# Kernel optimization log

Measured on AMD Instinct MI355X. Metric: run time of the kernel, lower is better.

## Reference

```python
import jax, jax.numpy as jnp
import numpy as np

N, T, HW = 32, 46, 128
VOCAB_Q, NUM_ANS = 96, 32
WVEC, RNN_DIM = 32, 128
CNN_DIM, G_DIM, F_DIM = 24, 256, 256
G_IN = 2 * (CNN_DIM + 2) + RNN_DIM  # 180
BN_EPS = 1e-5


def setup_inputs() -> dict:
    key = jax.random.key(0)
    ks = jax.random.split(key, 16)
    s = 0.05
    rn = lambda k, shape: jax.random.normal(k, shape, dtype=jnp.float32) * s
    z = lambda shape: jnp.zeros(shape, jnp.float32)
    o = lambda shape: jnp.ones(shape, jnp.float32)
    inp = {}
    inp['questions'] = jax.random.randint(ks[0], (N, T), 1, VOCAB_Q)  # no NULL padding -> last step is the valid hidden state
    inp['images'] = jax.random.normal(ks[1], (N, 3, HW, HW), dtype=jnp.float32)
    inp['embed_W'] = rn(ks[2], (VOCAB_Q, WVEC))
    inp['lstm_Wih'] = rn(ks[3], (4 * RNN_DIM, WVEC))
    inp['lstm_Whh'] = rn(ks[4], (4 * RNN_DIM, RNN_DIM))
    inp['lstm_bih'] = z((4 * RNN_DIM,))
    inp['lstm_bhh'] = z((4 * RNN_DIM,))
    inp['conv0_W'] = rn(ks[5], (CNN_DIM, 3, 3, 3))
    inp['conv0_b'] = z((CNN_DIM,))
    inp['bn0_g'] = o((CNN_DIM,))
    inp['bn0_b'] = z((CNN_DIM,))
    inp['convs_W'] = rn(ks[6], (3, CNN_DIM, CNN_DIM, 3, 3))
    inp['convs_b'] = z((3, CNN_DIM))
    inp['bns_g'] = o((3, CNN_DIM))
    inp['bns_b'] = z((3, CNN_DIM))
    inp['g0_W'] = rn(ks[7], (G_DIM, G_IN))
    inp['g0_b'] = z((G_DIM,))
    inp['gs_W'] = rn(ks[8], (3, G_DIM, G_DIM))
    inp['gs_b'] = z((3, G_DIM))
    inp['f0_W'] = rn(ks[9], (F_DIM, G_DIM))
    inp['f0_b'] = z((F_DIM,))
    inp['f1_W'] = rn(ks[10], (F_DIM, F_DIM))
    inp['f1_b'] = z((F_DIM,))
    inp['f2_W'] = rn(ks[11], (NUM_ANS, F_DIM))
    inp['f2_b'] = z((NUM_ANS,))
    return inp


def _dense(x, W, b):
    return x @ W.T + b


def _lstm_last(emb, Wih, Whh, bih, bhh):
    # emb: (N, T, D); single-layer LSTM, PyTorch gate order (i, f, g, o); return last hidden state
    n, h = emb.shape[0], Whh.shape[1]
    bias = bih + bhh

    def step(carry, x_t):
        hp, cp = carry
        zg = x_t @ Wih.T + hp @ Whh.T + bias
        i, f, g, o_ = jnp.split(zg, 4, axis=-1)
        c = jax.nn.sigmoid(f) * cp + jax.nn.sigmoid(i) * jnp.tanh(g)
        hn = jax.nn.sigmoid(o_) * jnp.tanh(c)
        return (hn, c), None

    init = (jnp.zeros((n, h), emb.dtype), jnp.zeros((n, h), emb.dtype))
    (h_last, _), _ = jax.lax.scan(step, init, jnp.swapaxes(emb, 0, 1))
    return h_last


def _conv_bn_relu(x, W, b, gamma, beta):
    # Conv2d(k=3, s=2, p=1) + BatchNorm2d (training-mode batch stats) + ReLU
    x = jax.lax.conv_general_dilated(x, W, window_strides=(2, 2), padding=((1, 1), (1, 1)),
                                     dimension_numbers=('NCHW', 'OIHW', 'NCHW'))
    x = x + b[None, :, None, None]
    mu = x.mean((0, 2, 3), keepdims=True)
    var = ((x - mu) ** 2).mean((0, 2, 3), keepdims=True)  # biased var, as torch BN
    x = (x - mu) * jax.lax.rsqrt(var + BN_EPS)
    x = x * gamma[None, :, None, None] + beta[None, :, None, None]
    return jax.nn.relu(x)


def _forward(questions, images, embed_W, lstm_Wih, lstm_Whh, lstm_bih, lstm_bhh,
             conv0_W, conv0_b, bn0_g, bn0_b, convs_W, convs_b, bns_g, bns_b,
             g0_W, g0_b, gs_W, gs_b, f0_W, f0_b, f1_W, f1_b, f2_W, f2_b):
    # question encoder
    q_feats = _lstm_last(embed_W[questions], lstm_Wih, lstm_Whh, lstm_bih, lstm_bhh)  # (N, rnn_dim)
    # CNN stem
    x = _conv_bn_relu(images, conv0_W, conv0_b, bn0_g, bn0_b)
    for i in range(3):
        x = _conv_bn_relu(x, convs_W[i], convs_b[i], bns_g[i], bns_b[i])
    n, c, h, w = x.shape
    m = h * w
    # append normalized coordinates
    xc = jnp.broadcast_to(jnp.linspace(0.0, 1.0, w, dtype=x.dtype).reshape(1, 1, 1, w), (n, 1, h, w))
    yc = jnp.broadcast_to(jnp.linspace(0.0, 1.0, h, dtype=x.dtype).reshape(1, 1, h, 1), (n, 1, h, w))
    objects = jnp.concatenate([x, xc, yc], axis=1).reshape(n, c + 2, m)
    objects = jnp.swapaxes(objects, 1, 2)  # (N, M, C+2)
    # all M^2 ordered pairs: pairs[n, i*M+j] = [obj_i, obj_j]
    feats1 = jnp.repeat(objects, m, axis=1)        # (N, M^2, C+2)
    feats2 = jnp.tile(objects, (1, m, 1))          # (N, M^2, C+2)
    q_rep = jnp.broadcast_to(q_feats[:, None, :], (n, m * m, q_feats.shape[-1]))
    g_in = jnp.concatenate([feats1, feats2, q_rep], axis=-1)  # (N, M^2, 180)
    # shared MLP g
    hidden = jax.nn.relu(_dense(g_in, g0_W, g0_b))
    for i in range(3):
        hidden = jax.nn.relu(_dense(hidden, gs_W[i], gs_b[i]))
    f_in = hidden.sum(axis=1)  # old-torch sum(1) kept dim then [:,0] -> (N, g_dim)
    # MLP f (dropout = identity at eval)
    hidden = jax.nn.relu(_dense(f_in, f0_W, f0_b))
    hidden = jax.nn.relu(_dense(hidden, f1_W, f1_b))
    return _dense(hidden, f2_W, f2_b)  # (N, num_answers)


def reference(questions, images, embed_W, lstm_Wih, lstm_Whh, lstm_bih, lstm_bhh,
              conv0_W, conv0_b, bn0_g, bn0_b, convs_W, convs_b, bns_g, bns_b,
              g0_W, g0_b, gs_W, gs_b, f0_W, f0_b, f1_W, f1_b, f2_W, f2_b):
    return _forward(questions, images, embed_W, lstm_Wih, lstm_Whh, lstm_bih, lstm_bhh,
                    conv0_W, conv0_b, bn0_g, bn0_b, convs_W, convs_b, bns_g, bns_b,
                    g0_W, g0_b, gs_W, gs_b, f0_W, f0_b, f1_W, f1_b, f2_W, f2_b)
```

## Files before the change

### kernel.cpp

```cpp
#include <hip/hip_runtime.h>

#define NB   32
#define TT   46
#define RNN  128
#define CDIM 24
#define GD   256
#define GIN  180

typedef __attribute__((ext_vector_type(8))) short  bf16x8;
typedef __attribute__((ext_vector_type(4))) short  s16x4;
typedef __attribute__((ext_vector_type(8))) unsigned short u16x8;
typedef __attribute__((ext_vector_type(4))) float  f32x4;

__device__ __forceinline__ unsigned short f2bf(float v) {
    unsigned u = __float_as_uint(v);
    u = u + 0x7fffu + ((u >> 16) & 1u);
    return (unsigned short)(u >> 16);
}

__device__ __forceinline__ float fast_sigmoid(float x) {
    return 1.f / (1.f + __expf(-x));
}
__device__ __forceinline__ float fast_tanh(float x) {
    return 1.f - 2.f / (__expf(2.f * x) + 1.f);
}

__device__ __forceinline__ void lstm_body(
    const int* __restrict__ q, const float* __restrict__ embW,
    const float* __restrict__ Wih, const float* __restrict__ Whh,
    const float* __restrict__ bih, const float* __restrict__ bhh,
    float* __restrict__ qf, int n)
{
    const int tid = threadIdx.x;
    __shared__ __align__(16) float xs[32], hs[RNN];
    __shared__ float zg[512];
    f32x4 wih[8], whh[32];
    {
        const f32x4* wp = (const f32x4*)(Wih + tid * 32);
#pragma unroll
        for (int j = 0; j < 8; j++) wih[j] = wp[j];
        const f32x4* hp = (const f32x4*)(Whh + tid * RNN);
#pragma unroll
        for (int j = 0; j < 32; j++) whh[j] = hp[j];
    }
    const float bias = bih[tid] + bhh[tid];
    float creg = 0.f;
    if (tid < RNN) hs[tid] = 0.f;
    float xr = (tid < 32) ? embW[q[n * TT] * 32 + tid] : 0.f;
    __syncthreads();
    for (int t = 0; t < TT; t++) {
        if (tid < 32) xs[tid] = xr;
        __syncthreads();
        if (tid < 32 && t + 1 < TT) xr = embW[q[n * TT + t + 1] * 32 + tid];
        const f32x4* h4 = (const f32x4*)hs;
        const f32x4* x4 = (const f32x4*)xs;
        f32x4 a0 = {0.f, 0.f, 0.f, 0.f}, a1 = a0, a2 = a0, a3 = a0;
#pragma unroll
        for (int j = 0; j < 8; j += 4) {
            a0 += wih[j] * x4[j];     a1 += wih[j + 1] * x4[j + 1];
            a2 += wih[j + 2] * x4[j + 2]; a3 += wih[j + 3] * x4[j + 3];
        }
#pragma unroll
        for (int j = 0; j < 32; j += 4) {
            a0 += whh[j] * h4[j];     a1 += whh[j + 1] * h4[j + 1];
            a2 += whh[j + 2] * h4[j + 2]; a3 += whh[j + 3] * h4[j + 3];
        }
        f32x4 a = (a0 + a1) + (a2 + a3);
        zg[tid] = bias + ((a[0] + a[1]) + (a[2] + a[3]));
        __syncthreads();
        if (tid < RNN) {
            float ig = fast_sigmoid(zg[tid]);
            float fg = fast_sigmoid(zg[RNN + tid]);
            float gg = fast_tanh(zg[2 * RNN + tid]);
            float og = fast_sigmoid(zg[3 * RNN + tid]);
            float cn = fg * creg + ig * gg;
            creg = cn;
            hs[tid] = og * fast_tanh(cn);
        }
        __syncthreads();
    }
    if (tid < RNN) qf[n * RNN + tid] = hs[tid];
}

template<int CIN, int TILE, bool BNIN, int BS>
__device__ __forceinline__ void conv_body(
    const float* __restrict__ in, const float* __restrict__ Wg,
    const float* __restrict__ bias,
    const float* __restrict__ pstats, const float* __restrict__ pg,
    const float* __restrict__ pb, float pinvM,
    float* __restrict__ out, float* __restrict__ stats,
    int HIN, int WIN, int HO, int WO, int tilesX, int bx)
{
    constexpr int NPIX = TILE * TILE;
    constexpr int CPG  = BS / NPIX;
    constexpr int COPT = 24 / CPG;
    constexpr int WPB  = BS / 64;
    constexpr int WPC  = NPIX / 64;
    constexpr int S  = 2 * TILE + 1;
    constexpr int SP = S + 1;
    __shared__ float in_t[CIN][S][SP];
    __shared__ float r1s[WPB][COPT], r2s[WPB][COPT];
    __shared__ float sc[CIN], sh[CIN];
    const int tid = threadIdx.x;
    const int tx = bx % tilesX;
    const int ty = (bx / tilesX) % tilesX;
    const int n  = bx / (tilesX * tilesX);

    if (BNIN) {
        if (tid < CIN) {
            float mu  = pstats[2 * tid] * pinvM;
            float var = pstats[2 * tid + 1] * pinvM - mu * mu;
            float rs  = rsqrtf(var + 1e-5f);
            sc[tid] = rs * pg[tid];
            sh[tid] = pb[tid] - mu * rs * pg[tid];
        }
        __syncthreads();
    }
    const int iy0 = ty * 2 * TILE - 1, ix0 = tx * 2 * TILE - 1;
    for (int idx = tid; idx < CIN * S * S; idx += BS) {
        int ci = idx / (S * S), r = idx % (S * S);
        int ry = r / S, rx = r % S;
        int gy = iy0 + ry, gx = ix0 + rx;
        float v = 0.f;
        if ((unsigned)gy < (unsigned)HIN && (unsigned)gx < (unsigned)WIN) {
            v = in[((size_t)(n * CIN + ci) * HIN + gy) * WIN + gx];
            if (BNIN) v = fmaxf(v * sc[ci] + sh[ci], 0.f);
        }
        in_t[ci][ry][rx] = v;
    }
    __syncthreads();

    const int p   = tid % NPIX;
    const int co0 = __builtin_amdgcn_readfirstlane((tid / NPIX) * COPT);
    const int ly  = (p / TILE) * 2, lx = (p % TILE) * 2;
    float acc[COPT];
#pragma unroll
    for (int c = 0; c < COPT; c++) acc[c] = bias[co0 + c];
    for (int ci = 0; ci < CIN; ci++) {
#pragma unroll
        for (int ky = 0; ky < 3; ky++) {
            const float* row = &in_t[ci][ly + ky][lx];
#pragma unroll
            for (int kx = 0; kx < 3; kx++) {
                float v = row[kx];
#pragma unroll
                for (int c = 0; c < COPT; c++)
                    acc[c] += v * Wg[(((co0 + c) * CIN + ci) * 3 + ky) * 3 + kx];
            }
        }
    }
    const int oy = ty * TILE + p / TILE, ox = tx * TILE + p % TILE;
#pragma unroll
    for (int c = 0; c < COPT; c++)
        out[((size_t)(n * 24 + co0 + c) * HO + oy) * WO + ox] = acc[c];

    const int lane = tid & 63, wv = tid >> 6;
#pragma unroll
    for (int c = 0; c < COPT; c++) {
        float s1 = acc[c], s2 = acc[c] * acc[c];
#pragma unroll
        for (int off = 1; off < 64; off <<= 1) {
            s1 += __shfl_xor(s1, off, 64);
            s2 += __shfl_xor(s2, off, 64);
        }
        if (lane == 0) { r1s[wv][c] = s1; r2s[wv][c] = s2; }
    }
    __syncthreads();
    if (tid < 24) {
        int cg = tid / COPT, slot = tid % COPT;
        float t1 = 0.f, t2 = 0.f;
#pragma unroll
        for (int u = 0; u < WPC; u++) { t1 += r1s[cg * WPC + u][slot]; t2 += r2s[cg * WPC + u][slot]; }
        atomicAdd(&stats[tid * 2],     t1);
        atomicAdd(&stats[tid * 2 + 1], t2);
    }
}

template<int CIN, int TILE, bool BNIN>
__global__ __launch_bounds__(256) void conv_tiled(
    const float* __restrict__ in, const float* __restrict__ Wg,
    const float* __restrict__ bias,
    const float* __restrict__ pstats, const float* __restrict__ pg,
    const float* __restrict__ pb, float pinvM,
    float* __restrict__ out, float* __restrict__ stats,
    int HIN, int WIN, int HO, int WO, int tilesX)
{
    conv_body<CIN, TILE, BNIN, 256>(in, Wg, bias, pstats, pg, pb, pinvM,
                                    out, stats, HIN, WIN, HO, WO, tilesX, blockIdx.x);
}

__global__ __launch_bounds__(512, 1) void fused_front(
    const int* __restrict__ q, const float* __restrict__ embW,
    const float* __restrict__ Wih, const float* __restrict__ Whh,
    const float* __restrict__ bih, const float* __restrict__ bhh,
    float* __restrict__ qf,
    const float* __restrict__ images, const float* __restrict__ c0W,
    const float* __restrict__ c0b, float* __restrict__ conv0o,
    float* __restrict__ stats,
    const float* __restrict__ gsW, unsigned short* __restrict__ Wbf)
{
    const int bx = blockIdx.x;
    if (bx < 32) {
        lstm_body(q, embW, Wih, Whh, bih, bhh, qf, bx);
    } else if (bx < 544) {
        conv_body<3, 16, false, 512>(images, c0W, c0b, nullptr, nullptr, nullptr, 0.f,
                                     conv0o, stats, 128, 128, 64, 64, 4, bx - 32);
    } else {
        int i = ((bx - 544) << 9) + threadIdx.x;
#pragma unroll
        for (int u = 0; u < 4; u++) {
            Wbf[i] = f2bf(gsW[i]);
            i += 96 * 512;
        }
    }
}

__global__ __launch_bounds__(256) void abqt_kernel(
    const float* __restrict__ feat,
    const float* __restrict__ stats, const float* __restrict__ g,
    const float* __restrict__ b, float invM,
    const float* __restrict__ qf,
    const float* __restrict__ g0W,
    const float* __restrict__ g0b,
    float* __restrict__ A, float* __restrict__ Bm, float* __restrict__ QT)
{
    const int n = blockIdx.x >> 2, iq = blockIdx.x & 3, k = threadIdx.x;
    __shared__ float wAB[256][53];
    __shared__ float wq[64][128];
    __shared__ float obj[16][28];
    __shared__ float qs[RNN];
    __shared__ float sc[24], sh[24];
    if (k < 24) {
        float mu  = stats[2 * k] * invM;
        float var = stats[2 * k + 1] * invM - mu * mu;
        float rs  = rsqrtf(var + 1e-5f);
        sc[k] = rs * g[k];
        sh[k] = b[k] - mu * rs * g[k];
    }
    if (k >= 128) qs[k - 128] = qf[n * RNN + (k - 128)];
    for (int idx = k; idx < 256 * 52; idx += 256) {
        int kr = idx / 52, c = idx % 52;
        wAB[kr][c] = g0W[kr * GIN + c];
    }
    for (int idx = k; idx < 64 * 128; idx += 256) {
        int r = idx >> 7, d = idx & 127;
        wq[r][d] = g0W[(((iq << 6) + r)) * GIN + 52 + d];
    }
    __syncthreads();
    for (int idx = k; idx < 24 * 16; idx += 256) {
        int c = idx >> 4, il = idx & 15;
        int i = (iq << 4) + il;
        float v = feat[(n * CDIM + c) * 64 + i];
        obj[il][c] = fmaxf(v * sc[c] + sh[c], 0.f);
    }
    if (k < 16) {
        int i = (iq << 4) + k;
        obj[k][24] = (float)(i & 7)  * (1.f / 7.f);
        obj[k][25] = (float)(i >> 3) * (1.f / 7.f);
        obj[k][26] = 0.f; obj[k][27] = 0.f;
    }
    __syncthreads();
    if (k < 64) {
        int kr = (iq << 6) + k;
        float qv = g0b[kr];
#pragma unroll
        for (int d = 0; d < RNN; d++) qv += wq[k][d] * qs[d];
        QT[(n << 8) + kr] = qv;
    }
    float wA[26], wB[26];
#pragma unroll
    for (int c = 0; c < 26; c++) { wA[c] = wAB[k][c]; wB[c] = wAB[k][26 + c]; }
    for (int il = 0; il < 16; il++) {
        const f32x4* op = (const f32x4*)obj[il];
        f32x4 r0 = op[0], r1 = op[1], r2 = op[2], r3 = op[3],
              r4 = op[4], r5 = op[5], r6 = op[6];
        float a = 0.f, bb = 0.f;
#pragma unroll
        for (int p = 0; p < 4; p++) {
            a += wA[p] * r0[p] + wA[4 + p] * r1[p] + wA[8 + p] * r2[p]
               + wA[12 + p] * r3[p] + wA[16 + p] * r4[p] + wA[20 + p] * r5[p];
            bb += wB[p] * r0[p] + wB[4 + p] * r1[p] + wB[8 + p] * r2[p]
                + wB[12 + p] * r3[p] + wB[16 + p] * r4[p] + wB[20 + p] * r5[p];
        }
        a += wA[24] * r6[0] + wA[25] * r6[1];
        bb += wB[24] * r6[0] + wB[25] * r6[1];
        int i = (iq << 4) + il;
        A [(((n << 6) + i) << 8) + k] = a;
        Bm[(((n << 6) + i) << 8) + k] = bb;
    }
}

__global__ __launch_bounds__(256, 2) void gs_fused(
    const float* __restrict__ A, const float* __restrict__ Bm, const float* __restrict__ QT,
    const unsigned short* __restrict__ Wb,
    const float* __restrict__ gsb,
    float* __restrict__ partial)
{
    __shared__ __align__(16) unsigned short Xs[128 * 256];
    __shared__ float biasv[3][256];
    const int raw = blockIdx.x;
    const int bb = (raw & 7) * 128 + (raw >> 3);
    const int n = bb >> 5, ip = bb & 31, tid = threadIdx.x;
    const int lane = tid & 63, w = tid >> 6, l15 = lane & 15, lh = lane >> 4;

    biasv[0][tid] = gsb[tid];
    biasv[1][tid] = gsb[256 + tid];
    biasv[2][tid] = gsb[512 + tid];

    {
        const int g = tid & 31, c0 = g << 3;
        const f32x4* qtp = (const f32x4*)(QT + (n << 8) + c0);
        f32x4 qta = qtp[0], qtb = qtp[1];
        const f32x4* a0p = (const f32x4*)(A + (((n << 6) + ip * 2)     << 8) + c0);
        const f32x4* a1p = (const f32x4*)(A + (((n << 6) + ip * 2 + 1) << 8) + c0);
        f32x4 aq0a = a0p[0] + qta, aq0b = a0p[1] + qtb;
        f32x4 aq1a = a1p[0] + qta, aq1b = a1p[1] + qtb;
#pragma unroll
        for (int it = 0; it < 16; it++) {
            int r = (tid >> 5) + (it << 3);
            int j = r & 63;
            f32x4 aa = (it < 8) ? aq0a : aq1a;
            f32x4 ab = (it < 8) ? aq0b : aq1b;
            const f32x4* bp = (const f32x4*)(Bm + (((n << 6) + j) << 8) + c0);
            f32x4 b0 = bp[0], b1 = bp[1];
            u16x8 pk;
#pragma unroll
            for (int p = 0; p < 4; p++) {
                pk[p]     = f2bf(fmaxf(b0[p] + aa[p], 0.f));
                pk[p + 4] = f2bf(fmaxf(b1[p] + ab[p], 0.f));
            }
            *(u16x8*)((char*)Xs + r * 512 + ((g ^ (r & 7)) << 4)) = pk;
        }
    }

    f32x4 acc[4][8];
    const f32x4 zero4 = {0.f, 0.f, 0.f, 0.f};
    bf16x8 wa[4], wn[4], xa[8], xn[8];
    for (int layer = 0; layer < 3; layer++) {
#pragma unroll
        for (int tc = 0; tc < 4; tc++)
#pragma unroll
            for (int sl = 0; sl < 8; sl++) acc[tc][sl] = zero4;
        const unsigned short* wbase = Wb + (layer << 16)
                                    + (((w << 6) + l15) << 8) + (lh << 3);
#pragma unroll
        for (int tc = 0; tc < 4; tc++) wa[tc] = *(const bf16x8*)(wbase + (tc << 12));
        __syncthreads();
#pragma unroll
        for (int sl = 0; sl < 8; sl++) {
            int ar = (sl << 4) + l15;
            int au = lh ^ (ar & 7);
            xa[sl] = *(const bf16x8*)((const char*)Xs + ar * 512 + (au << 4));
        }
#pragma unroll
        for (int kb = 0; kb < 8; kb++) {
            if (kb < 7) {
#pragma unroll
                for (int tc = 0; tc < 4; tc++)
                    wn[tc] = *(const bf16x8*)(wbase + (tc << 12) + ((kb + 1) << 5));
#pragma unroll
                for (int sl = 0; sl < 8; sl++) {
                    int ar = (sl << 4) + l15;
                    int au = (((kb + 1) << 2) + lh) ^ (ar & 7);
                    xn[sl] = *(const bf16x8*)((const char*)Xs + ar * 512 + (au << 4));
                }
            }
#pragma unroll
            for (int tc = 0; tc < 4; tc++)
#pragma unroll
                for (int sl = 0; sl < 8; sl++)
                    acc[tc][sl] = __builtin_amdgcn_mfma_f32_16x16x32_bf16(
                        wa[tc], xa[sl], acc[tc][sl], 0, 0, 0);
            if (kb < 7) {
#pragma unroll
                for (int tc = 0; tc < 4; tc++) wa[tc] = wn[tc];
#pragma unroll
                for (int sl = 0; sl < 8; sl++) xa[sl] = xn[sl];
            }
        }
        if (layer < 2) {
            __syncthreads();
#pragma unroll
            for (int tc = 0; tc < 4; tc++) {
                int c0 = (w << 6) + (tc << 4) + (lh << 2);
                float b0 = biasv[layer][c0],     b1 = biasv[layer][c0 + 1];
                float b2 = biasv[layer][c0 + 2], b3 = biasv[layer][c0 + 3];
#pragma unroll
                for (int sl = 0; sl < 8; sl++) {
                    int row = (sl << 4) + l15;
                    s16x4 pk;
                    pk[0] = (short)f2bf(fmaxf(acc[tc][sl][0] + b0, 0.f));
                    pk[1] = (short)f2bf(fmaxf(acc[tc][sl][1] + b1, 0.f));
                    pk[2] = (short)f2bf(fmaxf(acc[tc][sl][2] + b2, 0.f));
                    pk[3] = (short)f2bf(fmaxf(acc[tc][sl][3] + b3, 0.f));
                    *(s16x4*)((char*)Xs + row * 512 + (((c0 >> 3) ^ (row & 7)) << 4)
                              + ((c0 & 7) << 1)) = pk;
                }
            }
        } else {
#pragma unroll
            for (int tc = 0; tc < 4; tc++) {
                int c0 = (w << 6) + (tc << 4) + (lh << 2);
                f32x4 cs;
#pragma unroll
                for (int p = 0; p < 4; p++) {
                    float bv = biasv[2][c0 + p];
                    float s = 0.f;
#pragma unroll
                    for (int sl = 0; sl < 8; sl++) s += fmaxf(acc[tc][sl][p] + bv, 0.f);
                    s += __shfl_xor(s, 1, 64);
                    s += __shfl_xor(s, 2, 64);
                    s += __shfl_xor(s, 4, 64);
                    s += __shfl_xor(s, 8, 64);
                    cs[p] = s;
                }
                if (l15 == 0) *(f32x4*)(partial + (size_t)bb * 256 + c0) = cs;
            }
        }
    }
}

__device__ __forceinline__ float dot256(const float* __restrict__ wr,
                                        const float* __restrict__ x)
{
    const f32x4* w4 = (const f32x4*)wr;
    const f32x4* x4 = (const f32x4*)x;
    f32x4 a0 = {0.f, 0.f, 0.f, 0.f}, a1 = a0, a2 = a0, a3 = a0;
#pragma unroll 8
    for (int c = 0; c < 64; c += 4) {
        f32x4 w0 = w4[c], w1 = w4[c + 1], w2 = w4[c + 2], w3 = w4[c + 3];
        f32x4 x0 = x4[c], x1 = x4[c + 1], x2 = x4[c + 2], x3 = x4[c + 3];
        a0 += w0 * x0; a1 += w1 * x1; a2 += w2 * x2; a3 += w3 * x3;
    }
    f32x4 a = (a0 + a1) + (a2 + a3);
    return (a[0] + a[1]) + (a[2] + a[3]);
}

__global__ __launch_bounds__(256) void f_mlp(
    const float* __restrict__ partial,
    const float* __restrict__ f0W, const float* __restrict__ f0b,
    const float* __restrict__ f1W, const float* __restrict__ f1b,
    const float* __restrict__ f2W, const float* __restrict__ f2b,
    float* __restrict__ out)
{
    const int n = blockIdx.x, k = threadIdx.x;
    __shared__ float fin[256], h1[256], h2[256];
    const float* pb = partial + (size_t)(n * 32) * 256 + k;
    float s0 = 0.f, s1 = 0.f, s2 = 0.f, s3 = 0.f;
#pragma unroll
    for (int b = 0; b < 32; b += 4) {
        s0 += pb[(b + 0) << 8];
        s1 += pb[(b + 1) << 8];
        s2 += pb[(b + 2) << 8];
        s3 += pb[(b + 3) << 8];
    }
    fin[k] = (s0 + s1) + (s2 + s3);
    __syncthreads();
    h1[k] = fmaxf(dot256(f0W + (k << 8), fin) + f0b[k], 0.f);
    __syncthreads();
    h2[k] = fmaxf(dot256(f1W + (k << 8), h1) + f1b[k], 0.f);
    __syncthreads();
    if (k < 32)
        out[(n << 5) + k] = dot256(f2W + (k << 8), h2) + f2b[k];
}

extern "C" void kernel_launch(void* const* d_in, const int* in_sizes, int n_in,
                              void* d_out, int out_size, void* d_ws, size_t ws_size,
                              hipStream_t stream)
{
    const int*   questions = (const int*)  d_in[0];
    const float* images = (const float*)d_in[1];
    const float* embW   = (const float*)d_in[2];
    const float* Wih    = (const float*)d_in[3];
    const float* Whh    = (const float*)d_in[4];
    const float* bih    = (const float*)d_in[5];
    const float* bhh    = (const float*)d_in[6];
    const float* c0W    = (const float*)d_in[7];
    const float* c0b    = (const float*)d_in[8];
    const float* bn0g   = (const float*)d_in[9];
    const float* bn0b   = (const float*)d_in[10];
    const float* csW    = (const float*)d_in[11];
    const float* csb    = (const float*)d_in[12];
    const float* bnsg   = (const float*)d_in[13];
    const float* bnsb   = (const float*)d_in[14];
    const float* g0W    = (const float*)d_in[15];
    const float* g0b    = (const float*)d_in[16];
    const float* gsW    = (const float*)d_in[17];
    const float* gsb    = (const float*)d_in[18];
    const float* f0W    = (const float*)d_in[19];
    const float* f0b    = (const float*)d_in[20];
    const float* f1W    = (const float*)d_in[21];
    const float* f1b    = (const float*)d_in[22];
    const float* f2W    = (const float*)d_in[23];
    const float* f2b    = (const float*)d_in[24];

    float* ws  = (float*)d_ws;
    float* out = (float*)d_out;

    float* conv0o = ws;
    float* conv1o = ws + 3145728;
    float* conv2o = ws + 3932160;
    float* conv3o = ws + 4128768;
    float* stats  = ws + 4177920;
    float* qf     = ws + 4178112;
    unsigned short* Wbf = (unsigned short*)(ws + 4182208);
    float* Abuf   = ws;
    float* Bbuf   = ws + 524288;
    float* QTb    = ws + 1048576;
    float* part   = ws + 1155072;

    hipMemsetAsync(stats, 0, 192 * sizeof(float), stream);

    fused_front<<<640, 512, 0, stream>>>(questions, embW, Wih, Whh, bih, bhh, qf,
                                         images, c0W, c0b, conv0o, stats, gsW, Wbf);
    conv_tiled<24, 8, true><<<512, 256, 0, stream>>>(
        conv0o, csW, csb, stats, bn0g, bn0b, 1.f / 131072.f,
        conv1o, stats + 48, 64, 64, 32, 32, 4);
    conv_tiled<24, 8, true><<<128, 256, 0, stream>>>(
        conv1o, csW + 5184, csb + 24, stats + 48, bnsg, bnsb, 1.f / 32768.f,
        conv2o, stats + 96, 32, 32, 16, 16, 2);
    conv_tiled<24, 8, true><<<32, 256, 0, stream>>>(
        conv2o, csW + 10368, csb + 48, stats + 96, bnsg + 24, bnsb + 24, 1.f / 8192.f,
        conv3o, stats + 144, 16, 16, 8, 8, 1);

    abqt_kernel<<<128, 256, 0, stream>>>(conv3o, stats + 144, bnsg + 48, bnsb + 48,
                                         1.f / 2048.f, qf, g0W, g0b, Abuf, Bbuf, QTb);
    gs_fused<<<1024, 256, 0, stream>>>(Abuf, Bbuf, QTb, Wbf, gsb, part);
    f_mlp<<<32, 256, 0, stream>>>(part, f0W, f0b, f1W, f1b, f2W, f2b, out);
}
```

Before: 274.0 us.

## Fuse conv1-3 and abqt into one persistent kernel with grid barriers

Measured after the change: 355.5 us. +29.7%, slower.

```diff
diff --git a/kernel.cpp b/kernel.cpp
--- a/kernel.cpp
+++ b/kernel.cpp
@@ -84,11 +84,11 @@
 
 template<int CIN, int TILE, bool BNIN, int BS>
 __device__ __forceinline__ void conv_body(
-    const float* __restrict__ in, const float* __restrict__ Wg,
+    const float* in, const float* __restrict__ Wg,
     const float* __restrict__ bias,
-    const float* __restrict__ pstats, const float* __restrict__ pg,
+    const float* pstats, const float* __restrict__ pg,
     const float* __restrict__ pb, float pinvM,
-    float* __restrict__ out, float* __restrict__ stats,
+    float* out, float* stats,
     int HIN, int WIN, int HO, int WO, int tilesX, int bx)
 {
     constexpr int NPIX = TILE * TILE;
@@ -108,8 +108,10 @@
 
     if (BNIN) {
         if (tid < CIN) {
-            float mu  = pstats[2 * tid] * pinvM;
-            float var = pstats[2 * tid + 1] * pinvM - mu * mu;
+            float s1 = atomicAdd((float*)&pstats[2 * tid], 0.f);
+            float s2 = atomicAdd((float*)&pstats[2 * tid + 1], 0.f);
+            float mu  = s1 * pinvM;
+            float var = s2 * pinvM - mu * mu;
             float rs  = rsqrtf(var + 1e-5f);
             sc[tid] = rs * pg[tid];
             sh[tid] = pb[tid] - mu * rs * pg[tid];
@@ -174,19 +176,7 @@
         atomicAdd(&stats[tid * 2],     t1);
         atomicAdd(&stats[tid * 2 + 1], t2);
     }
-}
-
-template<int CIN, int TILE, bool BNIN>
-__global__ __launch_bounds__(256) void conv_tiled(
-    const float* __restrict__ in, const float* __restrict__ Wg,
-    const float* __restrict__ bias,
-    const float* __restrict__ pstats, const float* __restrict__ pg,
-    const float* __restrict__ pb, float pinvM,
-    float* __restrict__ out, float* __restrict__ stats,
-    int HIN, int WIN, int HO, int WO, int tilesX)
-{
-    conv_body<CIN, TILE, BNIN, 256>(in, Wg, bias, pstats, pg, pb, pinvM,
-                                    out, stats, HIN, WIN, HO, WO, tilesX, blockIdx.x);
+    __syncthreads();
 }
 
 __global__ __launch_bounds__(512, 1) void fused_front(
@@ -215,24 +205,34 @@
     }
 }
 
-__global__ __launch_bounds__(256) void abqt_kernel(
-    const float* __restrict__ feat,
-    const float* __restrict__ stats, const float* __restrict__ g,
+__device__ __forceinline__ void gbar(unsigned* bar, unsigned target) {
+    __syncthreads();
+    if (threadIdx.x == 0) {
+        __threadfence();
+        atomicAdd(bar, 1u);
+        while (atomicAdd(bar, 0u) < target) __builtin_amdgcn_s_sleep(2);
+        __threadfence();
+    }
+    __syncthreads();
+}
+
+__device__ __forceinline__ void abqt_body(
+    const float* feat, const float* pstats, const float* __restrict__ g,
     const float* __restrict__ b, float invM,
-    const float* __restrict__ qf,
-    const float* __restrict__ g0W,
+    const float* __restrict__ qf, const float* __restrict__ g0W,
     const float* __restrict__ g0b,
-    float* __restrict__ A, float* __restrict__ Bm, float* __restrict__ QT)
-{
-    const int n = blockIdx.x >> 2, iq = blockIdx.x & 3, k = threadIdx.x;
+    float* A, float* Bm, float* QT, int bx)
+{
+    const int n = bx >> 2, iq = bx & 3, k = threadIdx.x;
     __shared__ float wAB[256][53];
-    __shared__ float wq[64][128];
     __shared__ float obj[16][28];
     __shared__ float qs[RNN];
     __shared__ float sc[24], sh[24];
     if (k < 24) {
-        float mu  = stats[2 * k] * invM;
-        float var = stats[2 * k + 1] * invM - mu * mu;
+        float s1 = atomicAdd((float*)&pstats[2 * k], 0.f);
+        float s2 = atomicAdd((float*)&pstats[2 * k + 1], 0.f);
+        float mu  = s1 * invM;
+        float var = s2 * invM - mu * mu;
         float rs  = rsqrtf(var + 1e-5f);
         sc[k] = rs * g[k];
         sh[k] = b[k] - mu * rs * g[k];
@@ -241,10 +241,6 @@
     for (int idx = k; idx < 256 * 52; idx += 256) {
         int kr = idx / 52, c = idx % 52;
         wAB[kr][c] = g0W[kr * GIN + c];
-    }
-    for (int idx = k; idx < 64 * 128; idx += 256) {
-        int r = idx >> 7, d = idx & 127;
-        wq[r][d] = g0W[(((iq << 6) + r)) * GIN + 52 + d];
     }
     __syncthreads();
     for (int idx = k; idx < 24 * 16; idx += 256) {
@@ -263,8 +259,9 @@
     if (k < 64) {
         int kr = (iq << 6) + k;
         float qv = g0b[kr];
-#pragma unroll
-        for (int d = 0; d < RNN; d++) qv += wq[k][d] * qs[d];
+        const float* wqr = g0W + kr * GIN + 52;
+#pragma unroll
+        for (int d = 0; d < RNN; d++) qv += wqr[d] * qs[d];
         QT[(n << 8) + kr] = qv;
     }
     float wA[26], wB[26];
@@ -288,6 +285,37 @@
         A [(((n << 6) + i) << 8) + k] = a;
         Bm[(((n << 6) + i) << 8) + k] = bb;
     }
+}
+
+__global__ __launch_bounds__(256, 1) void mid_fused(
+    const float* conv0o, const float* __restrict__ csW, const float* __restrict__ csb,
+    const float* __restrict__ bn0g, const float* __restrict__ bn0b,
+    const float* __restrict__ bnsg, const float* __restrict__ bnsb,
+    float* stats, unsigned* bar,
+    float* conv1o, float* conv2o, float* conv3o,
+    const float* __restrict__ qf, const float* __restrict__ g0W,
+    const float* __restrict__ g0b,
+    float* A, float* Bm, float* QT)
+{
+    const int bx = blockIdx.x;
+    conv_body<24, 8, true, 256>(conv0o, csW, csb, stats, bn0g, bn0b, 1.f / 131072.f,
+                                conv1o, stats + 48, 64, 64, 32, 32, 4, bx);
+    conv_body<24, 8, true, 256>(conv0o, csW, csb, stats, bn0g, bn0b, 1.f / 131072.f,
+                                conv1o, stats + 48, 64, 64, 32, 32, 4, bx + 256);
+    gbar(bar, 256);
+    if (bx < 128)
+        conv_body<24, 8, true, 256>(conv1o, csW + 5184, csb + 24, stats + 48,
+                                    bnsg, bnsb, 1.f / 32768.f,
+                                    conv2o, stats + 96, 32, 32, 16, 16, 2, bx);
+    gbar(bar, 512);
+    if (bx < 32)
+        conv_body<24, 8, true, 256>(conv2o, csW + 10368, csb + 48, stats + 96,
+                                    bnsg + 24, bnsb + 24, 1.f / 8192.f,
+                                    conv3o, stats + 144, 16, 16, 8, 8, 1, bx);
+    gbar(bar, 768);
+    if (bx < 128)
+        abqt_body(conv3o, stats + 144, bnsg + 48, bnsb + 48, 1.f / 2048.f,
+                  qf, g0W, g0b, A, Bm, QT, bx);
 }
 
 __global__ __launch_bounds__(256, 2) void gs_fused(
@@ -502,29 +530,21 @@
     float* conv2o = ws + 3932160;
     float* conv3o = ws + 4128768;
     float* stats  = ws + 4177920;
-    float* qf     = ws + 4178112;
-    unsigned short* Wbf = (unsigned short*)(ws + 4182208);
+    unsigned* bar = (unsigned*)(ws + 4178112);
+    float* qf     = ws + 4178176;
+    unsigned short* Wbf = (unsigned short*)(ws + 4182272);
     float* Abuf   = ws;
     float* Bbuf   = ws + 524288;
     float* QTb    = ws + 1048576;
     float* part   = ws + 1155072;
 
-    hipMemsetAsync(stats, 0, 192 * sizeof(float), stream);
+    hipMemsetAsync(stats, 0, 256 * sizeof(float), stream);
 
     fused_front<<<640, 512, 0, stream>>>(questions, embW, Wih, Whh, bih, bhh, qf,
                                          images, c0W, c0b, conv0o, stats, gsW, Wbf);
-    conv_tiled<24, 8, true><<<512, 256, 0, stream>>>(
-        conv0o, csW, csb, stats, bn0g, bn0b, 1.f / 131072.f,
-        conv1o, stats + 48, 64, 64, 32, 32, 4);
-    conv_tiled<24, 8, true><<<128, 256, 0, stream>>>(
-        conv1o, csW + 5184, csb + 24, stats + 48, bnsg, bnsb, 1.f / 32768.f,
-        conv2o, stats + 96, 32, 32, 16, 16, 2);
-    conv_tiled<24, 8, true><<<32, 256, 0, stream>>>(
-        conv2o, csW + 10368, csb + 48, stats + 96, bnsg + 24, bnsb + 24, 1.f / 8192.f,
-        conv3o, stats + 144, 16, 16, 8, 8, 1);
-
-    abqt_kernel<<<128, 256, 0, stream>>>(conv3o, stats + 144, bnsg + 48, bnsb + 48,
-                                         1.f / 2048.f, qf, g0W, g0b, Abuf, Bbuf, QTb);
+    mid_fused<<<256, 256, 0, stream>>>(conv0o, csW, csb, bn0g, bn0b, bnsg, bnsb,
+                                       stats, bar, conv1o, conv2o, conv3o,
+                                       qf, g0W, g0b, Abuf, Bbuf, QTb);
     gs_fused<<<1024, 256, 0, stream>>>(Abuf, Bbuf, QTb, Wbf, gsb, part);
     f_mlp<<<32, 256, 0, stream>>>(part, f0W, f0b, f1W, f1b, f2W, f2b, out);
 }
```

## Interleave LSTM gate rows per lane and cut per-step barriers with double buffering

Applied to the files above, without the earlier changes.

Result: slower. 465.7 us (+69.9%).

```diff
diff --git a/kernel.cpp b/kernel.cpp
--- a/kernel.cpp
+++ b/kernel.cpp
@@ -32,28 +32,29 @@
     float* __restrict__ qf, int n)
 {
     const int tid = threadIdx.x;
-    __shared__ __align__(16) float xs[32], hs[RNN];
-    __shared__ float zg[512];
+    const int gate = tid & 3, unit = tid >> 2;
+    const int row  = gate * RNN + unit;
+    const int lane = tid & 63, lq = lane & ~3;
+    __shared__ __align__(16) float xs[2][32], hs[2][RNN];
     f32x4 wih[8], whh[32];
     {
-        const f32x4* wp = (const f32x4*)(Wih + tid * 32);
+        const f32x4* wp = (const f32x4*)(Wih + row * 32);
 #pragma unroll
         for (int j = 0; j < 8; j++) wih[j] = wp[j];
-        const f32x4* hp = (const f32x4*)(Whh + tid * RNN);
+        const f32x4* hp = (const f32x4*)(Whh + row * RNN);
 #pragma unroll
         for (int j = 0; j < 32; j++) whh[j] = hp[j];
     }
-    const float bias = bih[tid] + bhh[tid];
+    const float bias = bih[row] + bhh[row];
     float creg = 0.f;
-    if (tid < RNN) hs[tid] = 0.f;
-    float xr = (tid < 32) ? embW[q[n * TT] * 32 + tid] : 0.f;
+    if (tid < RNN) { hs[0][tid] = 0.f; }
+    if (tid < 32)  { xs[0][tid] = embW[q[n * TT] * 32 + tid]; }
+    float xr = (tid < 32 && TT > 1) ? embW[q[n * TT + 1] * 32 + tid] : 0.f;
     __syncthreads();
     for (int t = 0; t < TT; t++) {
-        if (tid < 32) xs[tid] = xr;
-        __syncthreads();
-        if (tid < 32 && t + 1 < TT) xr = embW[q[n * TT + t + 1] * 32 + tid];
-        const f32x4* h4 = (const f32x4*)hs;
-        const f32x4* x4 = (const f32x4*)xs;
+        const int cur = t & 1, nxt = cur ^ 1;
+        const f32x4* h4 = (const f32x4*)hs[cur];
+        const f32x4* x4 = (const f32x4*)xs[cur];
         f32x4 a0 = {0.f, 0.f, 0.f, 0.f}, a1 = a0, a2 = a0, a3 = a0;
 #pragma unroll
         for (int j = 0; j < 8; j += 4) {
@@ -66,20 +67,25 @@
             a2 += whh[j + 2] * h4[j + 2]; a3 += whh[j + 3] * h4[j + 3];
         }
         f32x4 a = (a0 + a1) + (a2 + a3);
-        zg[tid] = bias + ((a[0] + a[1]) + (a[2] + a[3]));
-        __syncthreads();
-        if (tid < RNN) {
-            float ig = fast_sigmoid(zg[tid]);
-            float fg = fast_sigmoid(zg[RNN + tid]);
-            float gg = fast_tanh(zg[2 * RNN + tid]);
-            float og = fast_sigmoid(zg[3 * RNN + tid]);
+        float p = bias + ((a[0] + a[1]) + (a[2] + a[3]));
+        if (tid < 32) xs[nxt][tid] = xr;
+        if (tid < 32 && t + 2 < TT) xr = embW[q[n * TT + t + 2] * 32 + tid];
+        float p0 = __shfl(p, lq + 0, 64);
+        float p1 = __shfl(p, lq + 1, 64);
+        float p2 = __shfl(p, lq + 2, 64);
+        float p3 = __shfl(p, lq + 3, 64);
+        if (gate == 0) {
+            float ig = fast_sigmoid(p0);
+            float fg = fast_sigmoid(p1);
+            float gg = fast_tanh(p2);
+            float og = fast_sigmoid(p3);
             float cn = fg * creg + ig * gg;
             creg = cn;
-            hs[tid] = og * fast_tanh(cn);
+            hs[nxt][unit] = og * fast_tanh(cn);
         }
         __syncthreads();
     }
-    if (tid < RNN) qf[n * RNN + tid] = hs[tid];
+    if (tid < RNN) qf[n * RNN + tid] = hs[TT & 1][tid];
 }
 
 template<int CIN, int TILE, bool BNIN, int BS>
```
